# Performance work log

Measured on AMD Instinct MI355X. Metric: run time of the kernel, lower is better.

## Reference

```python
import jax, jax.numpy as jnp
import numpy as np

NP_, NA_ = 100000, 50000           # paper / author node counts
E_C, E_W, E_B = 200000, 100000, 100000  # cites, writes, written_by edges
IN_DIM, OUT_DIM, H, DK = 256, 256, 8, 32
SLOPE, EPS = 0.2, 1e-5


def leaky(x):
    return jnp.where(x >= 0, x, SLOPE * x)


def seg_softmax(scores, seg, n):
    # softmax over edges grouped by destination node (DGL edge_softmax)
    m = jax.ops.segment_max(scores, seg, num_segments=n)
    e = jnp.exp(scores - m[seg])
    z = jax.ops.segment_sum(e, seg, num_segments=n)
    return e / z[seg]


def setup_inputs() -> dict:
    key = jax.random.key(0)
    k = jax.random.split(key, 14)
    s = 1.0 / np.sqrt(IN_DIM)
    return {
        "h_paper": jax.random.normal(k[0], (NP_, IN_DIM), jnp.float32),
        "h_author": jax.random.normal(k[1], (NA_, IN_DIM), jnp.float32),
        "fc_W": jax.random.normal(k[2], (OUT_DIM, IN_DIM), jnp.float32) * s,
        "fce_W": jax.random.normal(k[3], (OUT_DIM, OUT_DIM), jnp.float32) * s,
        "edge_emb": jax.random.normal(k[4], (3, OUT_DIM), jnp.float32) * 0.1,
        "attn_l": jax.random.normal(k[5], (1, H, DK), jnp.float32) * 0.1,
        "attn_r": jax.random.normal(k[6], (1, H, DK), jnp.float32) * 0.1,
        "attn_e": jax.random.normal(k[7], (1, H, DK), jnp.float32) * 0.1,
        "gamma": jnp.ones((OUT_DIM,), jnp.float32),
        "beta": jnp.zeros((OUT_DIM,), jnp.float32),
        "cites_src": jax.random.randint(k[8], (E_C,), 0, NP_),
        "cites_dst": jax.random.randint(k[9], (E_C,), 0, NP_),
        "writes_src": jax.random.randint(k[10], (E_W,), 0, NA_),
        "writes_dst": jax.random.randint(k[11], (E_W,), 0, NP_),
        "wb_src": jax.random.randint(k[12], (E_B,), 0, NP_),
        "wb_dst": jax.random.randint(k[13], (E_B,), 0, NA_),
    }


def reference(h_paper, h_author, fc_W, fce_W, edge_emb, attn_l, attn_r, attn_e,
              gamma, beta, cites_src, cites_dst, writes_src, writes_dst,
              wb_src, wb_dst):
    # fc projection (dropout = identity at eval)
    hp = (h_paper @ fc_W.T).reshape(-1, H, DK)   # [NP,H,DK]
    ha = (h_author @ fc_W.T).reshape(-1, H, DK)  # [NA,H,DK]
    # relation/edge-type embedding term: [3,H]
    ee = ((edge_emb @ fce_W.T).reshape(-1, H, DK) * attn_e).sum(-1)
    el_p = (hp * attn_l).sum(-1)  # [NP,H]
    er_p = (hp * attn_r).sum(-1)
    el_a = (ha * attn_l).sum(-1)
    er_a = (ha * attn_r).sum(-1)
    # per-edge unnormalized attention, leaky_relu(u_add_v + edge term)
    a_c = leaky(el_p[cites_src] + er_p[cites_dst] + ee[0])   # [E_C,H]
    a_w = leaky(el_a[writes_src] + er_p[writes_dst] + ee[1])  # [E_W,H]
    a_b = leaky(el_p[wb_src] + er_a[wb_dst] + ee[2])          # [E_B,H]
    # global softmax per destination node across all incoming relations
    seg_p = jnp.concatenate([cites_dst, writes_dst])
    attn_p = seg_softmax(jnp.concatenate([a_c, a_w], 0), seg_p, NP_)
    attn_a = seg_softmax(a_b, wb_dst, NA_)
    # weighted scatter-sum aggregation (u_mul_e, sum) with cross_reducer=sum
    ft_p = jnp.concatenate([hp[cites_src], ha[writes_src]], 0)  # [E,H,DK]
    t_p = jax.ops.segment_sum(ft_p * attn_p[:, :, None], seg_p,
                              num_segments=NP_).reshape(NP_, OUT_DIM)
    t_a = jax.ops.segment_sum(hp[wb_src] * attn_a[:, :, None], wb_dst,
                              num_segments=NA_).reshape(NA_, OUT_DIM)

    def ln(x):
        mu = x.mean(-1, keepdims=True)
        v = ((x - mu) ** 2).mean(-1, keepdims=True)
        return (x - mu) / jnp.sqrt(v + EPS) * gamma + beta

    out_p = ln(leaky(t_p + hp.reshape(NP_, OUT_DIM)))
    out_a = ln(leaky(t_a + ha.reshape(NA_, OUT_DIM)))
    return out_p, out_a
```

## Files before the change

kernel.cpp:

```cpp
#include <hip/hip_runtime.h>
#include <hip/hip_bf16.h>

#define NPAPER 100000
#define NAUTH  50000
#define NROWS  150000
#define EC 200000
#define EW 100000
#define EB 100000
#define ETOT 400000
#define DIM 256
#define NH 8
#define SLOPE 0.2f
#define LN_EPS 1e-5f
#define MAXD 32

#define NT 2344
#define PROJ_GRID 512
#define TPB 5

typedef unsigned short u16;
typedef __attribute__((ext_vector_type(8))) short s16x8;
typedef __attribute__((ext_vector_type(4))) float f32x4;

__device__ __forceinline__ float lrelu(float x){ return x >= 0.f ? x : SLOPE * x; }
__device__ __forceinline__ u16 f2b(float f){
  __hip_bfloat16 b = __float2bfloat16(f);
  return *reinterpret_cast<u16*>(&b);
}
__device__ __forceinline__ float b2f(u16 u){
  union { unsigned int i; float f; } v; v.i = ((unsigned int)u) << 16; return v.f;
}

__global__ void fill_i32(int* __restrict__ p, int v, int n){
  int i = blockIdx.x * blockDim.x + threadIdx.x;
  int stride = gridDim.x * blockDim.x;
  for (; i < n; i += stride) p[i] = v;
}

__global__ void prep_kernel(const float* __restrict__ fcW, const float* __restrict__ fceW,
                            const float* __restrict__ eEmb, const float* __restrict__ attn_e,
                            u16* __restrict__ Wb, float* __restrict__ eew)
{
  const int blk = blockIdx.x, tid = threadIdx.x;
  if (blk < 64){
    int i = blk * 256 + tid;
    float4 v = reinterpret_cast<const float4*>(fcW)[i];
    ushort4 o; o.x = f2b(v.x); o.y = f2b(v.y); o.z = f2b(v.z); o.w = f2b(v.w);
    reinterpret_cast<ushort4*>(Wb)[i] = o;
  } else {
    int b = blk - 64;
    int rel = b / 16, cg = b % 16;
    int wid = tid >> 6, l = tid & 63;
    int h = cg >> 1;
    float4 e4 = *reinterpret_cast<const float4*>(eEmb + rel * DIM + l * 4);
    float acc = 0.f;
    #pragma unroll
    for (int cc = 0; cc < 4; cc++){
      int c = cg * 16 + wid * 4 + cc;
      float4 w4 = *reinterpret_cast<const float4*>(fceW + (size_t)c * DIM + l * 4);
      float d = w4.x*e4.x + w4.y*e4.y + w4.z*e4.z + w4.w*e4.w;
      acc += d * attn_e[c];
    }
    #pragma unroll
    for (int m = 32; m > 0; m >>= 1) acc += __shfl_xor(acc, m, 64);
    if (l == 0) atomicAdd(&eew[rel * NH + h], acc);
  }
}

__global__ __launch_bounds__(512) void proj_mfma(
    const float* __restrict__ hP, const float* __restrict__ hA,
    const u16* __restrict__ Wb,
    const float* __restrict__ attn_l, const float* __restrict__ attn_r,
    u16* __restrict__ out, float* __restrict__ el, float* __restrict__ er)
{
  const int tid = threadIdx.x;
  const int l = tid & 63, wid = tid >> 6;
  const int lrow = l & 15, g = l >> 4;
  __shared__ u16 xs[2][64 * 256];

  const int t0 = blockIdx.x * TPB;
  if (t0 >= NT) return;
  const int nt = min(TPB, NT - t0);

  s16x8 bW0[8], bW1[8];
  {
    const u16* b0 = Wb + (size_t)(32 * wid + lrow) * DIM + g * 8;
    const u16* b1 = b0 + 16 * DIM;
    #pragma unroll
    for (int k = 0; k < 8; k++){
      bW0[k] = *reinterpret_cast<const s16x8*>(b0 + k * 32);
      bW1[k] = *reinterpret_cast<const s16x8*>(b1 + k * 32);
    }
  }
  float4 al0 = *reinterpret_cast<const float4*>(attn_l + 32 * wid + g * 4);
  float4 al1 = *reinterpret_cast<const float4*>(attn_l + 32 * wid + 16 + g * 4);
  float4 ar0 = *reinterpret_cast<const float4*>(attn_r + 32 * wid + g * 4);
  float4 ar1 = *reinterpret_cast<const float4*>(attn_r + 32 * wid + 16 + g * 4);

  float4 v[8];
  #pragma unroll
  for (int it = 0; it < 8; it++){
    int i = tid + it * 512;
    int row = i >> 6, c4 = (i & 63) << 2;
    int gr = t0 * 64 + row; gr = gr < NROWS ? gr : NROWS - 1;
    const float* base = (gr < NPAPER) ? hP + (size_t)gr * DIM + c4
                                      : hA + (size_t)(gr - NPAPER) * DIM + c4;
    v[it] = *reinterpret_cast<const float4*>(base);
  }
  #pragma unroll
  for (int it = 0; it < 8; it++){
    int i = tid + it * 512;
    int row = i >> 6, c4 = (i & 63) << 2;
    ushort4 o; o.x = f2b(v[it].x); o.y = f2b(v[it].y); o.z = f2b(v[it].z); o.w = f2b(v[it].w);
    int byte = (row * 256 + c4) * 2;
    byte ^= (row & 7) << 4;
    *reinterpret_cast<ushort4*>((char*)&xs[0][0] + byte) = o;
  }
  __syncthreads();

  for (int i = 0; i < nt; i++){
    const int cur = i & 1;
    const bool more = (i + 1 < nt);
    const int r0 = (t0 + i) * 64;
    if (more){
      #pragma unroll
      for (int it = 0; it < 8; it++){
        int ii = tid + it * 512;
        int row = ii >> 6, c4 = (ii & 63) << 2;
        int gr = r0 + 64 + row; gr = gr < NROWS ? gr : NROWS - 1;
        const float* base = (gr < NPAPER) ? hP + (size_t)gr * DIM + c4
                                          : hA + (size_t)(gr - NPAPER) * DIM + c4;
        v[it] = *reinterpret_cast<const float4*>(base);
      }
    }
    f32x4 acc[4][2];
    #pragma unroll
    for (int mi = 0; mi < 4; mi++){
      acc[mi][0] = (f32x4){0.f,0.f,0.f,0.f};
      acc[mi][1] = (f32x4){0.f,0.f,0.f,0.f};
    }
    #pragma unroll
    for (int kk = 0; kk < 8; kk++){
      s16x8 aF[4];
      #pragma unroll
      for (int mi = 0; mi < 4; mi++){
        int row = mi * 16 + lrow;
        int byte = (row * 256 + kk * 32 + g * 8) * 2;
        byte ^= (row & 7) << 4;
        aF[mi] = *reinterpret_cast<const s16x8*>((const char*)&xs[cur][0] + byte);
      }
      #pragma unroll
      for (int mi = 0; mi < 4; mi++){
        acc[mi][0] = __builtin_amdgcn_mfma_f32_16x16x32_bf16(bW0[kk], aF[mi], acc[mi][0], 0, 0, 0);
        acc[mi][1] = __builtin_amdgcn_mfma_f32_16x16x32_bf16(bW1[kk], aF[mi], acc[mi][1], 0, 0, 0);
      }
    }
    #pragma unroll
    for (int mi = 0; mi < 4; mi++){
      int grow = r0 + mi * 16 + lrow;
      bool ok = grow < NROWS;
      if (ok){
        #pragma unroll
        for (int ni = 0; ni < 2; ni++){
          int col = 32 * wid + ni * 16 + g * 4;
          ushort4 o;
          o.x = f2b(acc[mi][ni][0]); o.y = f2b(acc[mi][ni][1]);
          o.z = f2b(acc[mi][ni][2]); o.w = f2b(acc[mi][ni][3]);
          *reinterpret_cast<ushort4*>(out + (size_t)grow * DIM + col) = o;
        }
      }
      float sl = acc[mi][0][0]*al0.x + acc[mi][0][1]*al0.y
               + acc[mi][0][2]*al0.z + acc[mi][0][3]*al0.w
               + acc[mi][1][0]*al1.x + acc[mi][1][1]*al1.y
               + acc[mi][1][2]*al1.z + acc[mi][1][3]*al1.w;
      float sr = acc[mi][0][0]*ar0.x + acc[mi][0][1]*ar0.y
               + acc[mi][0][2]*ar0.z + acc[mi][0][3]*ar0.w
               + acc[mi][1][0]*ar1.x + acc[mi][1][1]*ar1.y
               + acc[mi][1][2]*ar1.z + acc[mi][1][3]*ar1.w;
      sl += __shfl_xor(sl, 16, 64);  sl += __shfl_xor(sl, 32, 64);
      sr += __shfl_xor(sr, 16, 64);  sr += __shfl_xor(sr, 32, 64);
      if (ok && g == 0){
        el[(size_t)grow * NH + wid] = sl;
        er[(size_t)grow * NH + wid] = sr;
      }
    }
    if (more){
      #pragma unroll
      for (int it = 0; it < 8; it++){
        int ii = tid + it * 512;
        int row = ii >> 6, c4 = (ii & 63) << 2;
        ushort4 o; o.x = f2b(v[it].x); o.y = f2b(v[it].y); o.z = f2b(v[it].z); o.w = f2b(v[it].w);
        int byte = (row * 256 + c4) * 2;
        byte ^= (row & 7) << 4;
        *reinterpret_cast<ushort4*>((char*)&xs[1 - cur][0] + byte) = o;
      }
    }
    __syncthreads();
  }
}

__global__ void scatter_direct(const int* __restrict__ c_src, const int* __restrict__ c_dst,
                               const int* __restrict__ w_src, const int* __restrict__ w_dst,
                               const int* __restrict__ b_src, const int* __restrict__ b_dst,
                               int* __restrict__ cursor, int* __restrict__ eidx){
  int i = blockIdx.x * blockDim.x + threadIdx.x;
  int gd, pk;
  if (i < EC)           { gd = c_dst[i];                pk = c_src[i]; }
  else if (i < EC + EW) { gd = w_dst[i - EC];           pk = (w_src[i - EC] + NPAPER) | (1 << 20); }
  else if (i < ETOT)    { gd = NPAPER + b_dst[i - EC - EW]; pk = b_src[i - EC - EW] | (2 << 20); }
  else return;
  int pos = atomicAdd(&cursor[gd], 1);
  if (pos < MAXD) eidx[(size_t)gd * MAXD + pos] = pk;
}

template<int K>
__device__ __forceinline__ void proc_edges(
    const int* __restrict__ erow, int base, int cnt,
    const float* __restrict__ el, float er_h,
    float ee0, float ee1, float ee2,
    const u16* __restrict__ hprojb, int l, int h,
    float& ax, float& ay, float& az, float& aw, float& zl)
{
  int pk[K]; float w[K]; ushort4 u[K];
  #pragma unroll
  for (int j = 0; j < K; j++)
    pk[j] = erow[base + (j < cnt ? j : 0)];
  #pragma unroll
  for (int j = 0; j < K; j++){
    int gs = pk[j] & 0xFFFFF, rl = pk[j] >> 20;
    u[j] = *reinterpret_cast<const ushort4*>(hprojb + (size_t)gs * DIM + l * 4);
    float sc = el[(size_t)gs * NH + h] + er_h + (rl == 0 ? ee0 : (rl == 1 ? ee1 : ee2));
    w[j] = (j < cnt) ? __expf(lrelu(sc)) : 0.f;
  }
  #pragma unroll
  for (int j = 0; j < K; j++){
    zl += w[j];
    ax += w[j] * b2f(u[j].x); ay += w[j] * b2f(u[j].y);
    az += w[j] * b2f(u[j].z); aw += w[j] * b2f(u[j].w);
  }
}

__global__ __launch_bounds__(256) void agg_ln_kernel(
    const int* __restrict__ counts, const int* __restrict__ eidx,
    const u16* __restrict__ hprojb,
    const float* __restrict__ el, const float* __restrict__ er,
    const float* __restrict__ eew, const float* __restrict__ gamma,
    const float* __restrict__ beta, float* __restrict__ out)
{
  const int wid = threadIdx.x >> 6, l = threadIdx.x & 63;
  const int r = blockIdx.x * 4 + wid;
  if (r >= NROWS) return;
  const int h = l >> 3;
  const float er_h = er[(size_t)r * NH + h];
  const float ee0 = eew[h], ee1 = eew[NH + h], ee2 = eew[2*NH + h];
  const int deg = min(counts[r], MAXD);
  const int* erow = eidx + (size_t)r * MAXD;

  float ax = 0.f, ay = 0.f, az = 0.f, aw = 0.f, zl = 0.f;
  int base = 0;
  while (deg - base >= 8){
    proc_edges<8>(erow, base, 8, el, er_h, ee0, ee1, ee2, hprojb, l, h, ax, ay, az, aw, zl);
    base += 8;
  }
  int rem = deg - base;
  if (rem > 4)      proc_edges<8>(erow, base, rem, el, er_h, ee0, ee1, ee2, hprojb, l, h, ax, ay, az, aw, zl);
  else if (rem > 2) proc_edges<4>(erow, base, rem, el, er_h, ee0, ee1, ee2, hprojb, l, h, ax, ay, az, aw, zl);
  else if (rem > 0) proc_edges<2>(erow, base, rem, el, er_h, ee0, ee1, ee2, hprojb, l, h, ax, ay, az, aw, zl);

  float iz = (deg > 0) ? 1.f / zl : 0.f;
  ushort4 hr = *reinterpret_cast<const ushort4*>(hprojb + (size_t)r * DIM + l * 4);
  float x0 = lrelu(ax * iz + b2f(hr.x));
  float x1 = lrelu(ay * iz + b2f(hr.y));
  float x2 = lrelu(az * iz + b2f(hr.z));
  float x3 = lrelu(aw * iz + b2f(hr.w));
  float s = x0 + x1 + x2 + x3;
  float q = x0*x0 + x1*x1 + x2*x2 + x3*x3;
  #pragma unroll
  for (int m = 32; m > 0; m >>= 1){
    s += __shfl_xor(s, m, 64);
    q += __shfl_xor(q, m, 64);
  }
  float mu  = s * (1.f / DIM);
  float var = q * (1.f / DIM) - mu * mu;
  float inv = rsqrtf(var + LN_EPS);
  float4 g  = *reinterpret_cast<const float4*>(gamma + l * 4);
  float4 bt = *reinterpret_cast<const float4*>(beta + l * 4);
  float4 o;
  o.x = (x0 - mu) * inv * g.x + bt.x;
  o.y = (x1 - mu) * inv * g.y + bt.y;
  o.z = (x2 - mu) * inv * g.z + bt.z;
  o.w = (x3 - mu) * inv * g.w + bt.w;
  *reinterpret_cast<float4*>(out + (size_t)r * DIM + l * 4) = o;
}

extern "C" void kernel_launch(void* const* d_in, const int* in_sizes, int n_in,
                              void* d_out, int out_size, void* d_ws, size_t ws_size,
                              hipStream_t stream)
{
  const float* hP     = (const float*)d_in[0];
  const float* hA     = (const float*)d_in[1];
  const float* fcW    = (const float*)d_in[2];
  const float* fceW   = (const float*)d_in[3];
  const float* eEmb   = (const float*)d_in[4];
  const float* attn_l = (const float*)d_in[5];
  const float* attn_r = (const float*)d_in[6];
  const float* attn_e = (const float*)d_in[7];
  const float* gamma  = (const float*)d_in[8];
  const float* beta   = (const float*)d_in[9];
  const int* c_src  = (const int*)d_in[10];
  const int* c_dst  = (const int*)d_in[11];
  const int* w_src  = (const int*)d_in[12];
  const int* w_dst  = (const int*)d_in[13];
  const int* b_src  = (const int*)d_in[14];
  const int* b_dst  = (const int*)d_in[15];

  u16*   hprojb = (u16*)d_ws;
  float* el    = (float*)(hprojb + (size_t)NROWS * DIM);
  float* er    = el    + (size_t)NROWS * NH;
  float* eew   = er    + (size_t)NROWS * NH;
  int*   cursor= (int*)(eew + 32);
  int*   eidx  = cursor + NROWS;
  u16*   Wb    = (u16*)(eidx + (size_t)NROWS * MAXD);

  const int TB = 256;

  fill_i32<<<256, TB, 0, stream>>>((int*)eew, 0, 32 + NROWS);
  scatter_direct<<<(ETOT + TB - 1) / TB, TB, 0, stream>>>(c_src, c_dst, w_src, w_dst,
                                                          b_src, b_dst, cursor, eidx);

  prep_kernel<<<112, TB, 0, stream>>>(fcW, fceW, eEmb, attn_e, Wb, eew);
  proj_mfma<<<PROJ_GRID, 512, 0, stream>>>(hP, hA, Wb, attn_l, attn_r,
                                           hprojb, el, er);

  agg_ln_kernel<<<NROWS / 4, TB, 0, stream>>>(cursor, eidx, hprojb,
                                              el, er, eew, gamma, beta,
                                              (float*)d_out);
}
```

Baseline: 180.8 us.

## Load projection A-fragments directly from global memory, one 64-row tile per block

Removes the LDS staging and double-buffered persistent loop from the projection GEMM. Each 256-thread block now handles one 64-row tile and half of the output columns, and each lane loads its fp32 A-fragment straight from global memory and converts it to bf16 in registers. This drops the LDS writes and reads and the barriers. In exchange, each input row is now read by both column-half blocks, which doubles input traffic unless the second read hits in cache, and the lane access pattern (32 bytes per lane per row) is less coalesced than before.

```diff
diff --git a/kernel.cpp b/kernel.cpp
--- a/kernel.cpp
+++ b/kernel.cpp
@@ -15,8 +15,6 @@
 #define MAXD 32
 
 #define NT 2344
-#define PROJ_GRID 512
-#define TPB 5
 
 typedef unsigned short u16;
 typedef __attribute__((ext_vector_type(8))) short s16x8;
@@ -67,7 +65,7 @@
   }
 }
 
-__global__ __launch_bounds__(512) void proj_mfma(
+__global__ __launch_bounds__(256) void proj_mfma(
     const float* __restrict__ hP, const float* __restrict__ hA,
     const u16* __restrict__ Wb,
     const float* __restrict__ attn_l, const float* __restrict__ attn_r,
@@ -76,15 +74,14 @@
   const int tid = threadIdx.x;
   const int l = tid & 63, wid = tid >> 6;
   const int lrow = l & 15, g = l >> 4;
-  __shared__ u16 xs[2][64 * 256];
-
-  const int t0 = blockIdx.x * TPB;
-  if (t0 >= NT) return;
-  const int nt = min(TPB, NT - t0);
+  const int t = blockIdx.x >> 1, half = blockIdx.x & 1;
+  const int r0 = t * 64;
+  const int col0 = 128 * half + 32 * wid;
+  const int hidx = 4 * half + wid;
 
   s16x8 bW0[8], bW1[8];
   {
-    const u16* b0 = Wb + (size_t)(32 * wid + lrow) * DIM + g * 8;
+    const u16* b0 = Wb + (size_t)(col0 + lrow) * DIM + g * 8;
     const u16* b1 = b0 + 16 * DIM;
     #pragma unroll
     for (int k = 0; k < 8; k++){
@@ -92,110 +89,76 @@
       bW1[k] = *reinterpret_cast<const s16x8*>(b1 + k * 32);
     }
   }
-  float4 al0 = *reinterpret_cast<const float4*>(attn_l + 32 * wid + g * 4);
-  float4 al1 = *reinterpret_cast<const float4*>(attn_l + 32 * wid + 16 + g * 4);
-  float4 ar0 = *reinterpret_cast<const float4*>(attn_r + 32 * wid + g * 4);
-  float4 ar1 = *reinterpret_cast<const float4*>(attn_r + 32 * wid + 16 + g * 4);
-
-  float4 v[8];
-  #pragma unroll
-  for (int it = 0; it < 8; it++){
-    int i = tid + it * 512;
-    int row = i >> 6, c4 = (i & 63) << 2;
-    int gr = t0 * 64 + row; gr = gr < NROWS ? gr : NROWS - 1;
-    const float* base = (gr < NPAPER) ? hP + (size_t)gr * DIM + c4
-                                      : hA + (size_t)(gr - NPAPER) * DIM + c4;
-    v[it] = *reinterpret_cast<const float4*>(base);
-  }
-  #pragma unroll
-  for (int it = 0; it < 8; it++){
-    int i = tid + it * 512;
-    int row = i >> 6, c4 = (i & 63) << 2;
-    ushort4 o; o.x = f2b(v[it].x); o.y = f2b(v[it].y); o.z = f2b(v[it].z); o.w = f2b(v[it].w);
-    int byte = (row * 256 + c4) * 2;
-    byte ^= (row & 7) << 4;
-    *reinterpret_cast<ushort4*>((char*)&xs[0][0] + byte) = o;
-  }
-  __syncthreads();
-
-  for (int i = 0; i < nt; i++){
-    const int cur = i & 1;
-    const bool more = (i + 1 < nt);
-    const int r0 = (t0 + i) * 64;
-    if (more){
+  float4 al0 = *reinterpret_cast<const float4*>(attn_l + col0 + g * 4);
+  float4 al1 = *reinterpret_cast<const float4*>(attn_l + col0 + 16 + g * 4);
+  float4 ar0 = *reinterpret_cast<const float4*>(attn_r + col0 + g * 4);
+  float4 ar1 = *reinterpret_cast<const float4*>(attn_r + col0 + 16 + g * 4);
+
+  const float* rowp[4];
+  #pragma unroll
+  for (int mi = 0; mi < 4; mi++){
+    int gr = r0 + mi * 16 + lrow;
+    int grc = gr < NROWS ? gr : NROWS - 1;
+    rowp[mi] = ((grc < NPAPER) ? hP + (size_t)grc * DIM
+                               : hA + (size_t)(grc - NPAPER) * DIM) + g * 8;
+  }
+
+  f32x4 acc[4][2];
+  #pragma unroll
+  for (int mi = 0; mi < 4; mi++){
+    acc[mi][0] = (f32x4){0.f,0.f,0.f,0.f};
+    acc[mi][1] = (f32x4){0.f,0.f,0.f,0.f};
+  }
+
+  #pragma unroll
+  for (int kk = 0; kk < 8; kk++){
+    s16x8 aF[4];
+    #pragma unroll
+    for (int mi = 0; mi < 4; mi++){
+      f32x4 a0 = *reinterpret_cast<const f32x4*>(rowp[mi] + kk * 32);
+      f32x4 a1 = *reinterpret_cast<const f32x4*>(rowp[mi] + kk * 32 + 4);
+      s16x8 af;
+      af[0] = (short)f2b(a0[0]); af[1] = (short)f2b(a0[1]);
+      af[2] = (short)f2b(a0[2]); af[3] = (short)f2b(a0[3]);
+      af[4] = (short)f2b(a1[0]); af[5] = (short)f2b(a1[1]);
+      af[6] = (short)f2b(a1[2]); af[7] = (short)f2b(a1[3]);
+      aF[mi] = af;
+    }
+    #pragma unroll
+    for (int mi = 0; mi < 4; mi++){
+      acc[mi][0] = __builtin_amdgcn_mfma_f32_16x16x32_bf16(bW0[kk], aF[mi], acc[mi][0], 0, 0, 0);
+      acc[mi][1] = __builtin_amdgcn_mfma_f32_16x16x32_bf16(bW1[kk], aF[mi], acc[mi][1], 0, 0, 0);
+    }
+  }
+
+  #pragma unroll
+  for (int mi = 0; mi < 4; mi++){
+    int grow = r0 + mi * 16 + lrow;
+    bool ok = grow < NROWS;
+    if (ok){
       #pragma unroll
-      for (int it = 0; it < 8; it++){
-        int ii = tid + it * 512;
-        int row = ii >> 6, c4 = (ii & 63) << 2;
-        int gr = r0 + 64 + row; gr = gr < NROWS ? gr : NROWS - 1;
-        const float* base = (gr < NPAPER) ? hP + (size_t)gr * DIM + c4
-                                          : hA + (size_t)(gr - NPAPER) * DIM + c4;
-        v[it] = *reinterpret_cast<const float4*>(base);
+      for (int ni = 0; ni < 2; ni++){
+        int col = col0 + ni * 16 + g * 4;
+        ushort4 o;
+        o.x = f2b(acc[mi][ni][0]); o.y = f2b(acc[mi][ni][1]);
+        o.z = f2b(acc[mi][ni][2]); o.w = f2b(acc[mi][ni][3]);
+        *reinterpret_cast<ushort4*>(out + (size_t)grow * DIM + col) = o;
       }
     }
-    f32x4 acc[4][2];
-    #pragma unroll
-    for (int mi = 0; mi < 4; mi++){
-      acc[mi][0] = (f32x4){0.f,0.f,0.f,0.f};
-      acc[mi][1] = (f32x4){0.f,0.f,0.f,0.f};
-    }
-    #pragma unroll
-    for (int kk = 0; kk < 8; kk++){
-      s16x8 aF[4];
-      #pragma unroll
-      for (int mi = 0; mi < 4; mi++){
-        int row = mi * 16 + lrow;
-        int byte = (row * 256 + kk * 32 + g * 8) * 2;
-        byte ^= (row & 7) << 4;
-        aF[mi] = *reinterpret_cast<const s16x8*>((const char*)&xs[cur][0] + byte);
-      }
-      #pragma unroll
-      for (int mi = 0; mi < 4; mi++){
-        acc[mi][0] = __builtin_amdgcn_mfma_f32_16x16x32_bf16(bW0[kk], aF[mi], acc[mi][0], 0, 0, 0);
-        acc[mi][1] = __builtin_amdgcn_mfma_f32_16x16x32_bf16(bW1[kk], aF[mi], acc[mi][1], 0, 0, 0);
-      }
-    }
-    #pragma unroll
-    for (int mi = 0; mi < 4; mi++){
-      int grow = r0 + mi * 16 + lrow;
-      bool ok = grow < NROWS;
-      if (ok){
-        #pragma unroll
-        for (int ni = 0; ni < 2; ni++){
-          int col = 32 * wid + ni * 16 + g * 4;
-          ushort4 o;
-          o.x = f2b(acc[mi][ni][0]); o.y = f2b(acc[mi][ni][1]);
-          o.z = f2b(acc[mi][ni][2]); o.w = f2b(acc[mi][ni][3]);
-          *reinterpret_cast<ushort4*>(out + (size_t)grow * DIM + col) = o;
-        }
-      }
-      float sl = acc[mi][0][0]*al0.x + acc[mi][0][1]*al0.y
-               + acc[mi][0][2]*al0.z + acc[mi][0][3]*al0.w
-               + acc[mi][1][0]*al1.x + acc[mi][1][1]*al1.y
-               + acc[mi][1][2]*al1.z + acc[mi][1][3]*al1.w;
-      float sr = acc[mi][0][0]*ar0.x + acc[mi][0][1]*ar0.y
-               + acc[mi][0][2]*ar0.z + acc[mi][0][3]*ar0.w
-               + acc[mi][1][0]*ar1.x + acc[mi][1][1]*ar1.y
-               + acc[mi][1][2]*ar1.z + acc[mi][1][3]*ar1.w;
-      sl += __shfl_xor(sl, 16, 64);  sl += __shfl_xor(sl, 32, 64);
-      sr += __shfl_xor(sr, 16, 64);  sr += __shfl_xor(sr, 32, 64);
-      if (ok && g == 0){
-        el[(size_t)grow * NH + wid] = sl;
-        er[(size_t)grow * NH + wid] = sr;
-      }
-    }
-    if (more){
-      #pragma unroll
-      for (int it = 0; it < 8; it++){
-        int ii = tid + it * 512;
-        int row = ii >> 6, c4 = (ii & 63) << 2;
-        ushort4 o; o.x = f2b(v[it].x); o.y = f2b(v[it].y); o.z = f2b(v[it].z); o.w = f2b(v[it].w);
-        int byte = (row * 256 + c4) * 2;
-        byte ^= (row & 7) << 4;
-        *reinterpret_cast<ushort4*>((char*)&xs[1 - cur][0] + byte) = o;
-      }
-    }
-    __syncthreads();
+    float sl = acc[mi][0][0]*al0.x + acc[mi][0][1]*al0.y
+             + acc[mi][0][2]*al0.z + acc[mi][0][3]*al0.w
+             + acc[mi][1][0]*al1.x + acc[mi][1][1]*al1.y
+             + acc[mi][1][2]*al1.z + acc[mi][1][3]*al1.w;
+    float sr = acc[mi][0][0]*ar0.x + acc[mi][0][1]*ar0.y
+             + acc[mi][0][2]*ar0.z + acc[mi][0][3]*ar0.w
+             + acc[mi][1][0]*ar1.x + acc[mi][1][1]*ar1.y
+             + acc[mi][1][2]*ar1.z + acc[mi][1][3]*ar1.w;
+    sl += __shfl_xor(sl, 16, 64);  sl += __shfl_xor(sl, 32, 64);
+    sr += __shfl_xor(sr, 16, 64);  sr += __shfl_xor(sr, 32, 64);
+    if (ok && g == 0){
+      el[(size_t)grow * NH + hidx] = sl;
+      er[(size_t)grow * NH + hidx] = sr;
+    }
   }
 }
 
@@ -329,8 +292,8 @@
                                                           b_src, b_dst, cursor, eidx);
 
   prep_kernel<<<112, TB, 0, stream>>>(fcW, fceW, eEmb, attn_e, Wb, eew);
-  proj_mfma<<<PROJ_GRID, 512, 0, stream>>>(hP, hA, Wb, attn_l, attn_r,
-                                           hprojb, el, er);
+  proj_mfma<<<2 * NT, TB, 0, stream>>>(hP, hA, Wb, attn_l, attn_r,
+                                       hprojb, el, er);
 
   agg_ln_kernel<<<NROWS / 4, TB, 0, stream>>>(cursor, eidx, hprojb,
                                               el, er, eew, gamma, beta,
```

Result: slower. 313.3 us (+73.3%).
